# Optimization experiments

Measured on AMD Instinct MI355X. Metric: run time of the kernel, lower is better.

The kernel has to match this reference:

```python
import jax, jax.numpy as jnp
import numpy as np

B, N, S, K = 16, 4, 64, 50        # batch, n_answers, q_len, n_boxes
VD, QD, H = 1024, 768, 512        # v_dim, q_dim, num_hid


def setup_inputs() -> dict:
    key = jax.random.key(0)
    ks = jax.random.split(key, 10)
    inp = {
        "v": jax.random.normal(ks[0], (B, 1, K, VD), dtype=jnp.float32),
        "q": jax.random.normal(ks[1], (B, N, S, 1, QD), dtype=jnp.float32),
        "box_mask": jax.random.randint(ks[2], (B, K), 0, 2, dtype=jnp.int32),
        "tags_attention": jax.random.normal(ks[3], (B, K), dtype=jnp.float32),
        # learned params (nn.Linear stores weight as [out, in])
        "Wv": jax.random.normal(ks[4], (H, VD), dtype=jnp.float32) * 0.02,
        "bv": jnp.zeros((H,), dtype=jnp.float32),
        "Wq": jax.random.normal(ks[5], (H, QD), dtype=jnp.float32) * 0.02,
        "bq": jnp.zeros((H,), dtype=jnp.float32),
        "Wl": jax.random.normal(ks[6], (1, H), dtype=jnp.float32) * 0.02,
        "bl": jnp.zeros((1,), dtype=jnp.float32),
    }
    return inp


def reference(v, q, box_mask, tags_attention, Wv, bv, Wq, bq, Wl, bl):
    # v_proj = Linear(v).unsqueeze(1): [B,1,K,H] -> [B,1,1,K,H]
    v_proj = (jnp.einsum('bokd,hd->bokh', v, Wv) + bv)[:, None]
    # q_proj: [B,N,S,1,H]
    q_proj = jnp.einsum('bnsod,hd->bnsoh', q, Wq) + bq
    # broadcast add + tanh: joint_repr [B,N,S,K,H] (the big intermediate)
    joint_repr = jnp.tanh(v_proj + q_proj)
    # score reduce over H: logits [B,N,S,K]
    logits = jnp.einsum('bnskh,oh->bnsko', joint_repr, Wl)[..., 0] + bl[0]
    # masked softmax over boxes with mask box_mask[:,None,None] -> [B,1,1,K]
    mask = (box_mask > 0)[:, None, None]
    w = jax.nn.softmax(jnp.where(mask, logits, jnp.float32(-1e9)), axis=-1)
    return w
```

## Files before the change

kernel.cpp:

```cpp
#include <hip/hip_runtime.h>
#include <hip/hip_bf16.h>
#include <cstddef>


typedef __attribute__((ext_vector_type(2))) float        f32x2;
typedef __attribute__((ext_vector_type(4))) float        f32x4;
typedef __attribute__((ext_vector_type(8))) short        bfrag;
typedef __attribute__((ext_vector_type(4))) unsigned int u32x4;

#define LGKM0  asm volatile("s_waitcnt lgkmcnt(0)" ::: "memory")
#define SBAR   __builtin_amdgcn_s_barrier()
#define SCHED0 __builtin_amdgcn_sched_barrier(0)

__device__ __forceinline__ void gload4(const float* g, float* l) {
  __builtin_amdgcn_global_load_lds((const __attribute__((address_space(1))) void*)g,
                                   (__attribute__((address_space(3))) void*)l, 4, 0, 0);
}

__device__ __forceinline__ unsigned int cvtpk(float a, float b) {
  unsigned int r;
  asm("v_cvt_pk_bf16_f32 %0, %1, %2" : "=v"(r) : "v"(a), "v"(b));
  return r;
}

template<int CTRL>
__device__ __forceinline__ float dpp_add(float x) {
  int r = __builtin_amdgcn_update_dpp(0, __float_as_int(x), CTRL, 0xF, 0xF, false);
  return x + __int_as_float(r);
}

__global__ void __launch_bounds__(256) gemm_fused(
    const float* __restrict__ v,  const float* __restrict__ q,
    const float* __restrict__ Wv, const float* __restrict__ bv,
    const float* __restrict__ Wq, const float* __restrict__ bq,
    float* __restrict__ vpw, float* __restrict__ qpw) {
  __shared__ unsigned short As[2][64 * 64];
  __shared__ unsigned short Bs[2][64 * 64];

  const int id = blockIdx.x;
  const int m  = (id & 7) + ((id >> 6) << 3);
  const int nt = (id >> 3) & 7;
  if (m >= 77) return;

  const int t = threadIdx.x;

  const float* A; const float* W; const float* bias; float* C;
  int M, Kd, m0;
  if (m < 13) { A = v; W = Wv; bias = bv; C = vpw; M = 800;  Kd = 1024; m0 = m * 64; }
  else        { A = q; W = Wq; bias = bq; C = qpw; M = 4096; Kd = 768;  m0 = (m - 13) * 64; }
  const int n0 = nt * 64;

  const int lane = t & 63;
  const int wave = t >> 6;
  const int wm   = wave >> 1;
  const int wn   = wave & 1;
  const int la   = lane & 15;
  const int lb   = lane >> 4;

  const int srow = t >> 2;
  const int skq  = (t & 3) * 16;

  int gr = m0 + srow; if (gr >= M) gr = M - 1;
  const float* Arow = A + (size_t)gr * Kd + skq;
  const float* Wrow = W + (size_t)(n0 + srow) * Kd + skq;

  f32x4 acc[2][2] = {};
  f32x4 raA[4], rbA[4], raB[4], rbB[4];

  auto loadG = [&](f32x4* ra, f32x4* rb, int s) {
    const float* ap = Arow + s * 64;
    const float* wp = Wrow + s * 64;
#pragma unroll
    for (int i = 0; i < 4; ++i) ra[i] = *(const f32x4*)&ap[i * 4];
#pragma unroll
    for (int i = 0; i < 4; ++i) rb[i] = *(const f32x4*)&wp[i * 4];
  };

  const int o0 = (srow * 128 + skq * 2)      ^ ((srow & 7) << 4);
  const int o1 = (srow * 128 + skq * 2 + 16) ^ ((srow & 7) << 4);

  auto writeL = [&](unsigned short* da, unsigned short* db,
                    const f32x4* ra, const f32x4* rb) {
    u32x4 p;
    p[0] = cvtpk(ra[0][0], ra[0][1]); p[1] = cvtpk(ra[0][2], ra[0][3]);
    p[2] = cvtpk(ra[1][0], ra[1][1]); p[3] = cvtpk(ra[1][2], ra[1][3]);
    *(u32x4*)((char*)da + o0) = p;
    p[0] = cvtpk(ra[2][0], ra[2][1]); p[1] = cvtpk(ra[2][2], ra[2][3]);
    p[2] = cvtpk(ra[3][0], ra[3][1]); p[3] = cvtpk(ra[3][2], ra[3][3]);
    *(u32x4*)((char*)da + o1) = p;
    p[0] = cvtpk(rb[0][0], rb[0][1]); p[1] = cvtpk(rb[0][2], rb[0][3]);
    p[2] = cvtpk(rb[1][0], rb[1][1]); p[3] = cvtpk(rb[1][2], rb[1][3]);
    *(u32x4*)((char*)db + o0) = p;
    p[0] = cvtpk(rb[2][0], rb[2][1]); p[1] = cvtpk(rb[2][2], rb[2][3]);
    p[2] = cvtpk(rb[3][0], rb[3][1]); p[3] = cvtpk(rb[3][2], rb[3][3]);
    *(u32x4*)((char*)db + o1) = p;
  };

  auto compute = [&](const unsigned short* sa, const unsigned short* sb) {
    bfrag af[2][2], bf[2][2];
#pragma unroll
    for (int r = 0; r < 2; ++r)
#pragma unroll
      for (int kk = 0; kk < 2; ++kk) {
        int rowa = wm * 32 + r * 16 + la;
        af[r][kk] = *(const bfrag*)((const char*)sa +
                     ((rowa * 128 + kk * 64 + lb * 16) ^ ((rowa & 7) << 4)));
        int rowb = wn * 32 + r * 16 + la;
        bf[r][kk] = *(const bfrag*)((const char*)sb +
                     ((rowb * 128 + kk * 64 + lb * 16) ^ ((rowb & 7) << 4)));
      }
#pragma unroll
    for (int kk = 0; kk < 2; ++kk)
#pragma unroll
      for (int r = 0; r < 2; ++r)
#pragma unroll
        for (int c = 0; c < 2; ++c)
          acc[r][c] = __builtin_amdgcn_mfma_f32_16x16x32_bf16(af[r][kk], bf[c][kk], acc[r][c], 0, 0, 0);
  };

  const int nsteps = Kd >> 6;
  loadG(raA, rbA, 0);
  writeL(As[0], Bs[0], raA, rbA);
  loadG(raA, rbA, 1);
  loadG(raB, rbB, 2);
  LGKM0; SCHED0; SBAR; SCHED0;
  for (int s = 0; s < nsteps; s += 2) {
    compute(As[0], Bs[0]);
    SBAR; SCHED0;
    writeL(As[1], Bs[1], raA, rbA);
    if (s + 3 < nsteps) loadG(raA, rbA, s + 3);
    LGKM0; SCHED0; SBAR; SCHED0;
    compute(As[1], Bs[1]);
    SBAR; SCHED0;
    if (s + 2 < nsteps) {
      writeL(As[0], Bs[0], raB, rbB);
      if (s + 4 < nsteps) loadG(raB, rbB, s + 4);
      LGKM0; SCHED0;
    }
    SBAR; SCHED0;
  }

  const float CEXP = 2.885390081777927f;
#pragma unroll
  for (int c = 0; c < 2; ++c) {
    int col = n0 + wn * 32 + c * 16 + la;
    float bcol = bias[col];
#pragma unroll
    for (int r = 0; r < 2; ++r) {
      int mbase = m0 + wm * 32 + r * 16 + lb * 4;
#pragma unroll
      for (int e = 0; e < 4; ++e) {
        int mr = mbase + e;
        if (mr < M)
          C[(size_t)mr * 512 + col] =
              __builtin_amdgcn_exp2f((acc[r][c][e] + bcol) * CEXP);
      }
    }
  }
}

__global__ void
__attribute__((amdgpu_flat_work_group_size(1024, 1024), amdgpu_waves_per_eu(4, 4)))
stage3_kernel(
    const float* __restrict__ vp, const float* __restrict__ qp,
    const float* __restrict__ wl, const int* __restrict__ box_mask,
    float* __restrict__ out) {
  __shared__ float vpS[50][512];
  __shared__ float redS[16][64][4];

  const int b    = blockIdx.y;
  const int grp  = blockIdx.x;
  const int t    = threadIdx.x;
  const int wv   = t >> 6;
  const int lane = t & 63;
  const int rowg = b * 256 + grp * 16 + wv;

  const float* qrow = qp + (size_t)rowg * 512;
  f32x2 eqr[4], wlr[4];
#pragma unroll
  for (int j = 0; j < 4; ++j) {
    eqr[j] = *(const f32x2*)&qrow[j * 128 + 2 * lane];
    f32x2 w = *(const f32x2*)&wl[j * 128 + 2 * lane];
    wlr[j][0] = -2.f * w[0];
    wlr[j][1] = -2.f * w[1];
  }

  {
    float* vf = &vpS[0][0];
    const float* src = vp + (size_t)b * 25600;
    const int ub = wv * 64;
#pragma unroll
    for (int i = 0; i < 25; ++i)
      gload4(src + i * 1024 + t, vf + i * 1024 + ub);
  }
  __syncthreads();

  const int g  = lane >> 4;
  const int li = lane & 15;

#pragma unroll 1
  for (int kc = 0; kc < 5; ++kc) {
    float acc[10];
#pragma unroll
    for (int i = 0; i < 10; ++i) acc[i] = 0.f;

#pragma unroll
    for (int i = 0; i < 10; ++i) {
      const f32x2* vr = (const f32x2*)&vpS[kc * 10 + i][0];
#pragma unroll
      for (int j = 0; j < 4; ++j) {
        f32x2 v2 = vr[j * 64 + lane];
        acc[i] = fmaf(wlr[j][0], __builtin_amdgcn_rcpf(fmaf(v2[0], eqr[j][0], 1.f)), acc[i]);
        acc[i] = fmaf(wlr[j][1], __builtin_amdgcn_rcpf(fmaf(v2[1], eqr[j][1], 1.f)), acc[i]);
      }
    }

#pragma unroll
    for (int i = 0; i < 10; ++i) {
      int k = kc * 10 + i;
      float s = acc[i];
      s = dpp_add<0x128>(s);
      s = dpp_add<0x124>(s);
      s = dpp_add<0x122>(s);
      s = dpp_add<0x121>(s);
      if (li == (k & 15)) redS[wv][k][g] = s;
    }
  }

  const int k = lane;
  f32x4 rv = *(const f32x4*)&redS[wv][k][0];
  float logit = (rv[0] + rv[1]) + (rv[2] + rv[3]);

  int   msk = (k < 50) ? box_mask[b * 50 + k] : 0;
  float l   = (k < 50 && msk > 0) ? logit : -1e9f;

  float mx = l;
#pragma unroll
  for (int off = 32; off; off >>= 1) mx = fmaxf(mx, __shfl_xor(mx, off));
  float e = (k < 50) ? __builtin_amdgcn_exp2f((l - mx) * 1.4426950408889634f) : 0.f;
  float s = e;
#pragma unroll
  for (int off = 32; off; off >>= 1) s += __shfl_xor(s, off);

  if (k < 50) out[(size_t)rowg * 50 + k] = e / s;
}

extern "C" void kernel_launch(void* const* d_in, const int* in_sizes, int n_in,
                              void* d_out, int out_size, void* d_ws, size_t ws_size,
                              hipStream_t stream) {
  const float* v        = (const float*)d_in[0];
  const float* q        = (const float*)d_in[1];
  const int*   box_mask = (const int*)d_in[2];
  const float* Wv       = (const float*)d_in[4];
  const float* bv       = (const float*)d_in[5];
  const float* Wq       = (const float*)d_in[6];
  const float* bq       = (const float*)d_in[7];
  const float* Wl       = (const float*)d_in[8];
  float* out = (float*)d_out;

  char* ws = (char*)d_ws;
  float* vpw = (float*)(ws);
  float* qpw = (float*)(ws + 1638400);

  gemm_fused<<<dim3(640),     256,  0, stream>>>(v, q, Wv, bv, Wq, bq, vpw, qpw);
  stage3_kernel<<<dim3(16, 16), 1024, 0, stream>>>(vpw, qpw, Wl, box_mask, out);
}
```

Baseline: 49.52 us.

## Store exponentiated v projection as bf16 and stage it with 16-byte LDS loads

The GEMM epilogue now writes exp(2·v_proj) as bf16 instead of fp32. The attention kernel copies it into a half-size LDS tile using 16-byte global_load_lds per lane (one row per wave) instead of 4-byte loads. The inner loop reads four bf16 values per LDS access and widens them to fp32, with the q projection and Wl operands regrouped as float4. This cuts global write and read traffic, LDS footprint and load instruction count. The cost is bf16 rounding of the exponentiated value, which feeds the tanh and the logits.

```diff
diff --git a/kernel.cpp b/kernel.cpp
--- a/kernel.cpp
+++ b/kernel.cpp
@@ -3,18 +3,23 @@
 #include <cstddef>
 
 
-typedef __attribute__((ext_vector_type(2))) float        f32x2;
-typedef __attribute__((ext_vector_type(4))) float        f32x4;
-typedef __attribute__((ext_vector_type(8))) short        bfrag;
-typedef __attribute__((ext_vector_type(4))) unsigned int u32x4;
+typedef __attribute__((ext_vector_type(2))) float          f32x2;
+typedef __attribute__((ext_vector_type(4))) float          f32x4;
+typedef __attribute__((ext_vector_type(8))) short          bfrag;
+typedef __attribute__((ext_vector_type(4))) unsigned int   u32x4;
+typedef __attribute__((ext_vector_type(4))) unsigned short u16x4;
 
 #define LGKM0  asm volatile("s_waitcnt lgkmcnt(0)" ::: "memory")
 #define SBAR   __builtin_amdgcn_s_barrier()
 #define SCHED0 __builtin_amdgcn_sched_barrier(0)
 
-__device__ __forceinline__ void gload4(const float* g, float* l) {
+__device__ __forceinline__ void gload4(const void* g, void* l) {
   __builtin_amdgcn_global_load_lds((const __attribute__((address_space(1))) void*)g,
                                    (__attribute__((address_space(3))) void*)l, 4, 0, 0);
+}
+__device__ __forceinline__ void gload16(const void* g, void* l) {
+  __builtin_amdgcn_global_load_lds((const __attribute__((address_space(1))) void*)g,
+                                   (__attribute__((address_space(3))) void*)l, 16, 0, 0);
 }
 
 __device__ __forceinline__ unsigned int cvtpk(float a, float b) {
@@ -23,6 +28,10 @@
   return r;
 }
 
+__device__ __forceinline__ float bf2f(unsigned short u) {
+  return __uint_as_float((unsigned int)u << 16);
+}
+
 template<int CTRL>
 __device__ __forceinline__ float dpp_add(float x) {
   int r = __builtin_amdgcn_update_dpp(0, __float_as_int(x), CTRL, 0xF, 0xF, false);
@@ -33,7 +42,7 @@
     const float* __restrict__ v,  const float* __restrict__ q,
     const float* __restrict__ Wv, const float* __restrict__ bv,
     const float* __restrict__ Wq, const float* __restrict__ bq,
-    float* __restrict__ vpw, float* __restrict__ qpw) {
+    unsigned short* __restrict__ evw, float* __restrict__ qpw) {
   __shared__ unsigned short As[2][64 * 64];
   __shared__ unsigned short Bs[2][64 * 64];
 
@@ -44,10 +53,11 @@
 
   const int t = threadIdx.x;
 
-  const float* A; const float* W; const float* bias; float* C;
+  const float* A; const float* W; const float* bias;
   int M, Kd, m0;
-  if (m < 13) { A = v; W = Wv; bias = bv; C = vpw; M = 800;  Kd = 1024; m0 = m * 64; }
-  else        { A = q; W = Wq; bias = bq; C = qpw; M = 4096; Kd = 768;  m0 = (m - 13) * 64; }
+  const bool vpath = (m < 13);
+  if (vpath) { A = v; W = Wv; bias = bv; M = 800;  Kd = 1024; m0 = m * 64; }
+  else       { A = q; W = Wq; bias = bq; M = 4096; Kd = 768;  m0 = (m - 13) * 64; }
   const int n0 = nt * 64;
 
   const int lane = t & 63;
@@ -151,9 +161,11 @@
 #pragma unroll
       for (int e = 0; e < 4; ++e) {
         int mr = mbase + e;
-        if (mr < M)
-          C[(size_t)mr * 512 + col] =
-              __builtin_amdgcn_exp2f((acc[r][c][e] + bcol) * CEXP);
+        if (mr < M) {
+          float val = __builtin_amdgcn_exp2f((acc[r][c][e] + bcol) * CEXP);
+          if (vpath) evw[(size_t)mr * 512 + col] = (unsigned short)cvtpk(val, val);
+          else       qpw[(size_t)mr * 512 + col] = val;
+        }
       }
     }
   }
@@ -162,10 +174,10 @@
 __global__ void
 __attribute__((amdgpu_flat_work_group_size(1024, 1024), amdgpu_waves_per_eu(4, 4)))
 stage3_kernel(
-    const float* __restrict__ vp, const float* __restrict__ qp,
+    const unsigned short* __restrict__ ev, const float* __restrict__ qp,
     const float* __restrict__ wl, const int* __restrict__ box_mask,
     float* __restrict__ out) {
-  __shared__ float vpS[50][512];
+  __shared__ unsigned short vpS[50][512];
   __shared__ float redS[16][64][4];
 
   const int b    = blockIdx.y;
@@ -176,22 +188,22 @@
   const int rowg = b * 256 + grp * 16 + wv;
 
   const float* qrow = qp + (size_t)rowg * 512;
-  f32x2 eqr[4], wlr[4];
-#pragma unroll
-  for (int j = 0; j < 4; ++j) {
-    eqr[j] = *(const f32x2*)&qrow[j * 128 + 2 * lane];
-    f32x2 w = *(const f32x2*)&wl[j * 128 + 2 * lane];
-    wlr[j][0] = -2.f * w[0];
-    wlr[j][1] = -2.f * w[1];
+  f32x4 eqr[2], wlr[2];
+#pragma unroll
+  for (int j = 0; j < 2; ++j) {
+    eqr[j] = *(const f32x4*)&qrow[j * 256 + 4 * lane];
+    f32x4 w = *(const f32x4*)&wl[j * 256 + 4 * lane];
+#pragma unroll
+    for (int e = 0; e < 4; ++e) wlr[j][e] = -2.f * w[e];
   }
 
   {
-    float* vf = &vpS[0][0];
-    const float* src = vp + (size_t)b * 25600;
-    const int ub = wv * 64;
-#pragma unroll
-    for (int i = 0; i < 25; ++i)
-      gload4(src + i * 1024 + t, vf + i * 1024 + ub);
+    const unsigned short* src = ev + (size_t)b * 25600 + lane * 8;
+#pragma unroll
+    for (int i = 0; i < 4; ++i) {
+      int kr = i * 16 + wv;
+      if (kr < 50) gload16(src + kr * 512, &vpS[kr][0]);
+    }
   }
   __syncthreads();
 
@@ -206,13 +218,17 @@
 
 #pragma unroll
     for (int i = 0; i < 10; ++i) {
-      const f32x2* vr = (const f32x2*)&vpS[kc * 10 + i][0];
-#pragma unroll
-      for (int j = 0; j < 4; ++j) {
-        f32x2 v2 = vr[j * 64 + lane];
-        acc[i] = fmaf(wlr[j][0], __builtin_amdgcn_rcpf(fmaf(v2[0], eqr[j][0], 1.f)), acc[i]);
-        acc[i] = fmaf(wlr[j][1], __builtin_amdgcn_rcpf(fmaf(v2[1], eqr[j][1], 1.f)), acc[i]);
-      }
+      const unsigned short* vr = &vpS[kc * 10 + i][0];
+      u16x4 va = *(const u16x4*)&vr[4 * lane];
+      u16x4 vb = *(const u16x4*)&vr[256 + 4 * lane];
+#pragma unroll
+      for (int e = 0; e < 4; ++e)
+        acc[i] = fmaf(wlr[0][e],
+                      __builtin_amdgcn_rcpf(fmaf(bf2f(va[e]), eqr[0][e], 1.f)), acc[i]);
+#pragma unroll
+      for (int e = 0; e < 4; ++e)
+        acc[i] = fmaf(wlr[1][e],
+                      __builtin_amdgcn_rcpf(fmaf(bf2f(vb[e]), eqr[1][e], 1.f)), acc[i]);
     }
 
 #pragma unroll
@@ -259,9 +275,9 @@
   float* out = (float*)d_out;
 
   char* ws = (char*)d_ws;
-  float* vpw = (float*)(ws);
-  float* qpw = (float*)(ws + 1638400);
-
-  gemm_fused<<<dim3(640),     256,  0, stream>>>(v, q, Wv, bv, Wq, bq, vpw, qpw);
-  stage3_kernel<<<dim3(16, 16), 1024, 0, stream>>>(vpw, qpw, Wl, box_mask, out);
-}
+  float*          qpw = (float*)(ws);
+  unsigned short* evw = (unsigned short*)(ws + 8388608);
+
+  gemm_fused<<<dim3(640),     256,  0, stream>>>(v, q, Wv, bv, Wq, bq, evw, qpw);
+  stage3_kernel<<<dim3(16, 16), 1024, 0, stream>>>(evw, qpw, Wl, box_mask, out);
+}
```

After: 49.99 us. About the same (+1.0%).
